# Kernel tuning notes

Hardware: AMD Instinct MI355X
Metric: run time of the kernel (lower is better)

## Reference

```python
import jax, jax.numpy as jnp
import numpy as np

PRE_NMS_LIMIT = 6000
PROPOSAL_COUNT = 1000
NMS_THRESHOLD = 0.7
BBOX_STD = jnp.array([0.1, 0.1, 0.2, 0.2], dtype=jnp.float32)
NEG = -1e9  # suppressed-score sentinel


def setup_inputs() -> dict:
    key = jax.random.key(0)
    k1, k2, k3, k4 = jax.random.split(key, 4)
    B, N = 8, 262144
    rpn_probs = jax.random.uniform(k1, (B, N, 2), dtype=jnp.float32)
    rpn_bbox = jax.random.normal(k2, (B, N, 4), dtype=jnp.float32) * 0.1
    # anchors as valid (y1, x1, y2, x2) boxes in normalized coords
    cyx = jax.random.uniform(k3, (B, N, 2), dtype=jnp.float32)
    hw = jax.random.uniform(k4, (B, N, 2), dtype=jnp.float32, minval=0.02, maxval=0.3)
    anchors = jnp.concatenate([cyx - 0.5 * hw, cyx + 0.5 * hw], axis=-1)
    return {"rpn_probs": rpn_probs, "rpn_bbox": rpn_bbox, "anchors": anchors}


def _apply_deltas(a, d):
    # a, d: [K, 4]; a = (y1, x1, y2, x2); d = (dy, dx, log dh, log dw)
    h = a[:, 2] - a[:, 0]
    w = a[:, 3] - a[:, 1]
    cy = a[:, 0] + 0.5 * h + d[:, 0] * h
    cx = a[:, 1] + 0.5 * w + d[:, 1] * w
    h = h * jnp.exp(d[:, 2])
    w = w * jnp.exp(d[:, 3])
    return jnp.stack([cy - 0.5 * h, cx - 0.5 * w, cy + 0.5 * h, cx + 0.5 * w], axis=-1)


def _iou_one_vs_all(box, boxes):
    # box [4], boxes [K, 4]
    y1 = jnp.maximum(box[0], boxes[:, 0])
    x1 = jnp.maximum(box[1], boxes[:, 1])
    y2 = jnp.minimum(box[2], boxes[:, 2])
    x2 = jnp.minimum(box[3], boxes[:, 3])
    inter = jnp.maximum(y2 - y1, 0.0) * jnp.maximum(x2 - x1, 0.0)
    area_b = (box[2] - box[0]) * (box[3] - box[1])
    areas = (boxes[:, 2] - boxes[:, 0]) * (boxes[:, 3] - boxes[:, 1])
    return inter / (area_b + areas - inter + 1e-10)


def _nms(boxes, scores):
    # greedy NMS: boxes [K, 4], scores [K] -> padded [P, 4], [P]
    K = scores.shape[0]
    idx = jnp.arange(K)

    def step(scores_m, _):
        i = jnp.argmax(scores_m)
        s = scores_m[i]
        valid = s > 0.5 * NEG
        box = boxes[i]
        iou = _iou_one_vs_all(box, boxes)
        scores_m = jnp.where((iou > NMS_THRESHOLD) | (idx == i), NEG, scores_m)
        return scores_m, (jnp.where(valid, box, 0.0), jnp.where(valid, s, 0.0))

    _, (props, pscores) = jax.lax.scan(step, scores, None, length=PROPOSAL_COUNT)
    return props, pscores


def reference(rpn_probs, rpn_bbox, anchors):
    scores = rpn_probs[:, :, 1]                      # [B, N] fg prob
    deltas = rpn_bbox * BBOX_STD                      # [B, N, 4]
    k = min(PRE_NMS_LIMIT, anchors.shape[1])
    top_scores, ix = jax.lax.top_k(scores, k)         # [B, K]
    gather = jax.vmap(lambda x, i: x[i])
    d = gather(deltas, ix)                            # [B, K, 4]
    a = gather(anchors, ix)                           # [B, K, 4]
    boxes = jax.vmap(_apply_deltas)(a, d)             # [B, K, 4]
    boxes = jnp.clip(boxes, 0.0, 1.0)                 # clip to window [0,0,1,1]
    proposals, pscores = jax.vmap(_nms)(boxes, top_scores)
    return proposals, pscores
```

## Files before the change

kernel.cpp:

```cpp
#include <hip/hip_runtime.h>
#include <stdint.h>

#define BB 8
#define NN 262144
#define KSEL 6000
#define KPAD2 6144
#define NW2 24
#define PROP 1000
#define NMS_THR 0.7f
#define CAND_CAP 8192
#define BPB 64
#define STAGE_CAP 768
#define MAT_U64_PB 282624ull
#define DIAG_U64_PB 24576ull

__device__ __forceinline__ unsigned long long shfl_xor_u64(unsigned long long v, int m) {
    unsigned lo = (unsigned)v, hi = (unsigned)(v >> 32);
    lo = __shfl_xor(lo, m);
    hi = __shfl_xor(hi, m);
    return ((unsigned long long)hi << 32) | lo;
}
__device__ __forceinline__ uint64_t rdfl64(uint64_t v) {
    uint32_t lo = __builtin_amdgcn_readfirstlane((uint32_t)v);
    uint32_t hi = __builtin_amdgcn_readfirstlane((uint32_t)(v >> 32));
    return ((uint64_t)hi << 32) | lo;
}
__device__ __forceinline__ uint64_t rdlane64(uint64_t v, uint32_t l) {
    uint32_t lo = __builtin_amdgcn_readlane((uint32_t)v, l);
    uint32_t hi = __builtin_amdgcn_readlane((uint32_t)(v >> 32), l);
    return ((uint64_t)hi << 32) | lo;
}

__device__ __forceinline__ uint32_t sup_bit(const float4 bi, float ai, const float4 bj, float aj) {
    float y1 = fmaxf(bi.x, bj.x), x1 = fmaxf(bi.y, bj.y);
    float y2 = fminf(bi.z, bj.z), x2 = fminf(bi.w, bj.w);
    float inter = __fmul_rn(fmaxf(__fsub_rn(y2, y1), 0.f), fmaxf(__fsub_rn(x2, x1), 0.f));
    float den = __fadd_rn(__fsub_rn(__fadd_rn(ai, aj), inter), 1e-10f);
    const double MSUP = 23488103.0 / 33554432.0;
    return (double)inter >= MSUP * (double)den;
}

__device__ __forceinline__ uint32_t score_bin(float sc) {
    uint32_t u = (uint32_t)(sc * 16777216.0f);
    u = u > 16777215u ? 16777215u : u;
    return u >> 16;
}

__global__ void k_zero(uint32_t* __restrict__ ghist, uint32_t* __restrict__ cnt,
                       uint32_t* __restrict__ ncount, uint32_t* __restrict__ ndone) {
    int b = blockIdx.x, t = threadIdx.x;
    ghist[(b << 8) + t] = 0u;
    if (t == 0) { cnt[b] = 0u; ncount[b] = 0u; ndone[b] = 0u; }
}

__global__ void k_hist(const float4* __restrict__ probs, uint32_t* __restrict__ ghist) {
    __shared__ uint32_t lh[256];
    int blk = blockIdx.x;
    int b = blk >> 6;
    int t = threadIdx.x;
    lh[t] = 0u;
    __syncthreads();
    size_t fbase = ((size_t)b * (NN / 2)) + (size_t)(blk & 63) * 2048;
#pragma unroll
    for (int k = 0; k < 8; ++k) {
        float4 v = probs[fbase + k * 256 + t];
        atomicAdd(&lh[score_bin(v.y)], 1u);
        atomicAdd(&lh[score_bin(v.w)], 1u);
    }
    __syncthreads();
    uint32_t c = lh[t];
    if (c) atomicAdd(&ghist[(b << 8) + t], c);
}

__global__ void k_compact(const float4* __restrict__ probs, const uint32_t* __restrict__ ghist,
                          uint32_t* __restrict__ cnt, uint64_t* __restrict__ cand) {
    __shared__ uint64_t stage[STAGE_CAP];
    __shared__ uint32_t lh[256];
    __shared__ uint32_t s_bst, lcnt, lbase;
    int blk = blockIdx.x;
    int b = blk >> 6;
    int t = threadIdx.x;
    lh[t] = ghist[(b << 8) + t];
    if (t == 0) lcnt = 0u;
    __syncthreads();
    if (t == 0) {
        uint32_t cum = 0; uint32_t bst = 0;
        for (int c = 255; c >= 0; --c) {
            cum += lh[c];
            if (cum >= (uint32_t)KSEL) { bst = (uint32_t)c; break; }
        }
        s_bst = bst;
    }
    __syncthreads();
    uint32_t bst = s_bst;
    int ibase = (blk & 63) * 4096;
    size_t fbase = ((size_t)b * (NN / 2)) + (size_t)(blk & 63) * 2048;
#pragma unroll
    for (int k = 0; k < 8; ++k) {
        float4 v = probs[fbase + k * 256 + t];
        int i0 = ibase + (k * 256 + t) * 2;
#pragma unroll
        for (int e = 0; e < 2; ++e) {
            float sc = e ? v.w : v.y;
            if (score_bin(sc) >= bst) {
                uint32_t p = atomicAdd(&lcnt, 1u);
                if (p < STAGE_CAP) {
                    uint32_t bits = __float_as_uint(sc);
                    stage[p] = ((uint64_t)bits << 32) | (uint32_t)(~(uint32_t)(i0 + e));
                }
            }
        }
    }
    __syncthreads();
    if (t == 0) {
        uint32_t m = lcnt > STAGE_CAP ? STAGE_CAP : lcnt;
        lbase = atomicAdd(&cnt[b], m);
        lcnt = m;
    }
    __syncthreads();
    uint32_t m = lcnt, base = lbase;
    for (uint32_t s = t; s < m; s += 256) {
        uint32_t pos = base + s;
        if (pos < CAND_CAP) cand[((uint64_t)b << 13) + pos] = stage[s];
    }
}

__launch_bounds__(512)
__global__ void k_sort1(const uint32_t* __restrict__ cnt, uint64_t* __restrict__ cand) {
    __shared__ uint64_t key[1024];
    int b = blockIdx.y, ch = blockIdx.x, t = threadIdx.x;
    uint32_t M = cnt[b]; if (M > CAND_CAP) M = CAND_CAP;
    uint64_t* cb = cand + ((uint64_t)b << 13);
    int base = ch << 10;
    for (int i = t; i < 1024; i += 512) key[i] = ((uint32_t)(base + i) < M) ? cb[base + i] : 0ull;
    __syncthreads();
    for (int kk = 2; kk <= 1024; kk <<= 1) {
        for (int j = kk >> 1; j > 0; j >>= 1) {
            for (int e = t; e < 1024; e += 512) {
                int ixj = e ^ j;
                if (ixj > e) {
                    uint64_t a = key[e], c = key[ixj];
                    bool ddd = ((e & kk) == 0);
                    if ((a < c) == ddd) { key[e] = c; key[ixj] = a; }
                }
            }
            __syncthreads();
        }
    }
    for (int i = t; i < 1024; i += 512) cb[base + i] = key[i];
}

__launch_bounds__(256)
__global__ void k_merge(int R, const uint64_t* __restrict__ src, uint64_t* __restrict__ dst) {
    int b = blockIdx.y;
    int k = (blockIdx.x << 8) + threadIdx.x;
    const uint64_t* base = src + ((uint64_t)b << 13);
    int run = k / (2 * R);
    int ko = k - run * (2 * R);
    const uint64_t* A = base + (size_t)run * 2 * R;
    const uint64_t* B = A + R;
    int lo = ko - R; if (lo < 0) lo = 0;
    int hi = ko < R ? ko : R;
    while (lo < hi) {
        int m = (lo + hi) >> 1;
        int t = ko - m - 1;
        uint64_t bv = (t < 0) ? ~0ull : (t >= R ? 0ull : B[t]);
        if (A[m] > bv) lo = m + 1; else hi = m;
    }
    int i = lo, j = ko - lo;
    uint64_t av = (i >= R) ? 0ull : A[i];
    uint64_t bv = (j >= R) ? 0ull : B[j];
    dst[((uint64_t)b << 13) + k] = (av > bv) ? av : bv;
}

__launch_bounds__(256)
__global__ void k_merge_decode(const uint64_t* __restrict__ src,
                               const float4* __restrict__ rpn_bbox, const float4* __restrict__ anchors,
                               float4* __restrict__ boxes, float* __restrict__ scoresS,
                               float* __restrict__ areas) {
    const int R = 4096;
    int b = blockIdx.y;
    int k = (blockIdx.x << 8) + threadIdx.x;
    if (k >= KPAD2) return;
    const uint64_t* A = src + ((uint64_t)b << 13);
    const uint64_t* B = A + R;
    int lo = k - R; if (lo < 0) lo = 0;
    int hi = k < R ? k : R;
    while (lo < hi) {
        int m = (lo + hi) >> 1;
        int t = k - m - 1;
        uint64_t bv = (t < 0) ? ~0ull : (t >= R ? 0ull : B[t]);
        if (A[m] > bv) lo = m + 1; else hi = m;
    }
    int i = lo, j = k - lo;
    uint64_t av = (i >= R) ? 0ull : A[i];
    uint64_t bv = (j >= R) ? 0ull : B[j];
    uint64_t k64 = (av > bv) ? av : bv;

    float4 bx = make_float4(0.f, 0.f, 0.f, 0.f);
    float sc = 0.f, ar = 0.f;
    if (k < KSEL) {
        uint32_t idx = ~(uint32_t)(k64 & 0xFFFFFFFFull);
        sc = __uint_as_float((uint32_t)(k64 >> 32));
        size_t off = ((size_t)b << 18) + idx;
        float4 a = anchors[off];
        float4 d4 = rpn_bbox[off];
        float d0 = __fmul_rn(d4.x, 0.1f), d1 = __fmul_rn(d4.y, 0.1f);
        float d2 = __fmul_rn(d4.z, 0.2f), d3 = __fmul_rn(d4.w, 0.2f);
        float h = __fsub_rn(a.z, a.x), w = __fsub_rn(a.w, a.y);
        float cy = __fadd_rn(__fadd_rn(a.x, __fmul_rn(0.5f, h)), __fmul_rn(d0, h));
        float cx = __fadd_rn(__fadd_rn(a.y, __fmul_rn(0.5f, w)), __fmul_rn(d1, w));
        float h2 = __fmul_rn(h, expf(d2));
        float w2 = __fmul_rn(w, expf(d3));
        float y1 = __fsub_rn(cy, __fmul_rn(0.5f, h2));
        float x1 = __fsub_rn(cx, __fmul_rn(0.5f, w2));
        float y2 = __fadd_rn(cy, __fmul_rn(0.5f, h2));
        float x2 = __fadd_rn(cx, __fmul_rn(0.5f, w2));
        y1 = fminf(fmaxf(y1, 0.f), 1.f); x1 = fminf(fmaxf(x1, 0.f), 1.f);
        y2 = fminf(fmaxf(y2, 0.f), 1.f); x2 = fminf(fmaxf(x2, 0.f), 1.f);
        bx = make_float4(y1, x1, y2, x2);
        ar = __fmul_rn(__fsub_rn(y2, y1), __fsub_rn(x2, x1));
    }
    boxes[b * KPAD2 + k] = bx;
    scoresS[b * KPAD2 + k] = sc;
    areas[b * KPAD2 + k] = ar;
}

__launch_bounds__(256)
__global__ void k_matc(int w0, const float4* __restrict__ boxes, const float* __restrict__ areas,
                       uint64_t* __restrict__ mat, uint64_t* __restrict__ diag,
                       const uint32_t* __restrict__ done) {
    int b = blockIdx.y;
    if (done[b]) return;
    int q2 = blockIdx.x;
    int half = q2 & 1;
    int q = q2 >> 1, W = w0;
    while (q >= W + 1) { q -= W + 1; ++W; }
    int sub = q;
    int t = threadIdx.x;
    __shared__ float4 sb[128];
    __shared__ float sa[128];
    size_t bb = (size_t)b * KPAD2;
    int j0 = (W << 8) + (half << 7);
    if (t < 128) { sb[t] = boxes[bb + j0 + t]; sa[t] = areas[bb + j0 + t]; }
    __syncthreads();
    int i = (sub << 8) + t;
    float4 bi = boxes[bb + i];
    float ai = areas[bb + i];
    uint32_t a0 = 0, a1 = 0, a2 = 0, a3 = 0;
#pragma unroll 4
    for (int jj = 0; jj < 32; ++jj) {
        a0 |= sup_bit(bi, ai, sb[jj], sa[jj]) << jj;
        a1 |= sup_bit(bi, ai, sb[32 + jj], sa[32 + jj]) << jj;
        a2 |= sup_bit(bi, ai, sb[64 + jj], sa[64 + jj]) << jj;
        a3 |= sup_bit(bi, ai, sb[96 + jj], sa[96 + jj]) << jj;
    }
    uint64_t* row;
    if (sub == W) {
        row = diag + (uint64_t)b * DIAG_U64_PB + (uint64_t)(j0 & ~127) * 0
              + (uint64_t)((W << 8) + t) * 4;
    } else {
        row = mat + (uint64_t)b * MAT_U64_PB + 512ull * W * (W - 1) + (uint64_t)i * 4;
    }
    ulonglong2 v;
    v.x = (uint64_t)a0 | ((uint64_t)a1 << 32);
    v.y = (uint64_t)a2 | ((uint64_t)a3 << 32);
    *(ulonglong2*)(row + (half << 1)) = v;
}

__launch_bounds__(256)
__global__ void k_nms_chunk(int w0, int w1, int final_chunk,
                            const float4* __restrict__ boxes, const float* __restrict__ scoresS,
                            const uint64_t* __restrict__ diag, const uint64_t* __restrict__ mat,
                            uint32_t* __restrict__ gsel, uint32_t* __restrict__ ncount,
                            uint32_t* __restrict__ done, float* __restrict__ out) {
    __shared__ uint32_t sel[PROP];
    __shared__ uint64_t diagrow[256][4];
    __shared__ uint32_t suppw[8];
    __shared__ uint32_t s_count;

    int b = blockIdx.x;
    if (done[b]) return;
    int tid = threadIdx.x;
    int wid = tid >> 6, lane = tid & 63;
    size_t bb = (size_t)b * KPAD2;
    const uint64_t* mb = mat + (uint64_t)b * MAT_U64_PB;
    const uint64_t* dgb = diag + (uint64_t)b * DIAG_U64_PB;
    uint32_t* gs = gsel + b * 1024;

    int count = (int)ncount[b];
    for (int r = tid; r < count; r += 256) sel[r] = gs[r];
    __syncthreads();

    for (int W = w0; W < w1; ++W) {
        {
            const ulonglong2* src = (const ulonglong2*)(dgb + (uint64_t)(W << 8) * 4);
            ulonglong2* dst = (ulonglong2*)&diagrow[0][0];
            dst[tid * 2] = src[tid * 2];
            dst[tid * 2 + 1] = src[tid * 2 + 1];
        }
        if (tid < 8) suppw[tid] = 0u;
        __syncthreads();
        uint64_t acc0 = 0, acc1 = 0, acc2 = 0, acc3 = 0;
        {
            const uint64_t* col = mb + 512ull * W * (W - 1);
            uint32_t c = (uint32_t)count;
            uint32_t i0 = tid, i1 = tid + 256, i2 = tid + 512, i3 = tid + 768;
            if (i0 < c) { const ulonglong2* r = (const ulonglong2*)(col + 4u * sel[i0]);
                          ulonglong2 x = r[0], y = r[1];
                          acc0 |= x.x; acc1 |= x.y; acc2 |= y.x; acc3 |= y.y; }
            if (i1 < c) { const ulonglong2* r = (const ulonglong2*)(col + 4u * sel[i1]);
                          ulonglong2 x = r[0], y = r[1];
                          acc0 |= x.x; acc1 |= x.y; acc2 |= y.x; acc3 |= y.y; }
            if (i2 < c) { const ulonglong2* r = (const ulonglong2*)(col + 4u * sel[i2]);
                          ulonglong2 x = r[0], y = r[1];
                          acc0 |= x.x; acc1 |= x.y; acc2 |= y.x; acc3 |= y.y; }
            if (i3 < c) { const ulonglong2* r = (const ulonglong2*)(col + 4u * sel[i3]);
                          ulonglong2 x = r[0], y = r[1];
                          acc0 |= x.x; acc1 |= x.y; acc2 |= y.x; acc3 |= y.y; }
        }
#pragma unroll
        for (int off = 32; off; off >>= 1) {
            acc0 |= shfl_xor_u64(acc0, off);
            acc1 |= shfl_xor_u64(acc1, off);
            acc2 |= shfl_xor_u64(acc2, off);
            acc3 |= shfl_xor_u64(acc3, off);
        }
        if (lane == 0) {
            if (acc0) { atomicOr(&suppw[0], (uint32_t)acc0); atomicOr(&suppw[1], (uint32_t)(acc0 >> 32)); }
            if (acc1) { atomicOr(&suppw[2], (uint32_t)acc1); atomicOr(&suppw[3], (uint32_t)(acc1 >> 32)); }
            if (acc2) { atomicOr(&suppw[4], (uint32_t)acc2); atomicOr(&suppw[5], (uint32_t)(acc2 >> 32)); }
            if (acc3) { atomicOr(&suppw[6], (uint32_t)acc3); atomicOr(&suppw[7], (uint32_t)(acc3 >> 32)); }
        }
        __syncthreads();
        int count_old = count;
        if (wid == 0) {
            uint64_t a0 = ~(((uint64_t)suppw[1] << 32) | suppw[0]);
            uint64_t a1 = ~(((uint64_t)suppw[3] << 32) | suppw[2]);
            uint64_t a2 = ~(((uint64_t)suppw[5] << 32) | suppw[4]);
            uint64_t a3 = ~(((uint64_t)suppw[7] << 32) | suppw[6]);
            if (W == NW2 - 1) { a1 &= (1ull << 48) - 1; a2 = 0; a3 = 0; }
            uint64_t pk0 = 0, pk1 = 0, pk2 = 0, pk3 = 0;
            uint64_t hi_mask = (lane == 63) ? 0ull : (~0ull << (lane + 1));

#define SUBP(S, AS, PK)                                                       \
            if (AS && count < PROP) {                                         \
                uint64_t own = diagrow[(S << 6) + lane][S];                   \
                while (AS && count < PROP) {                                  \
                    uint32_t alive_l = (uint32_t)((AS >> lane) & 1ull);       \
                    uint64_t inter = own & AS & hi_mask;                      \
                    unsigned long long conf = __ballot(alive_l && (inter != 0ull)); \
                    uint64_t run, rowc = 0ull;                                \
                    if (conf == 0ull) { run = AS; }                           \
                    else {                                                    \
                        uint32_t c = (uint32_t)__builtin_ctzll(conf);         \
                        uint64_t lo = ((1ull << c) << 1) - 1ull;              \
                        run = AS & lo;                                        \
                        rowc = rdlane64(own, c);                              \
                    }                                                         \
                    int pr = (int)__popcll(run);                              \
                    if (count + pr > PROP) {                                  \
                        int need = PROP - count;                              \
                        while (need-- > 0) {                                  \
                            uint32_t bp = (uint32_t)__builtin_ctzll(run);     \
                            PK |= 1ull << bp;                                 \
                            run &= run - 1ull;                                \
                        }                                                     \
                        count = PROP; AS = 0ull;                              \
                    } else {                                                  \
                        PK |= run; count += pr;                               \
                        AS &= ~run; AS &= ~rowc;                              \
                    }                                                         \
                }                                                             \
            }
            SUBP(0, a0, pk0)
            if (pk0 && count < PROP) {
                uint32_t pl = (uint32_t)((pk0 >> lane) & 1ull);
                uint64_t x1 = pl ? diagrow[lane][1] : 0ull;
                uint64_t x2 = pl ? diagrow[lane][2] : 0ull;
                uint64_t x3 = pl ? diagrow[lane][3] : 0ull;
#pragma unroll
                for (int off = 32; off; off >>= 1) {
                    x1 |= shfl_xor_u64(x1, off);
                    x2 |= shfl_xor_u64(x2, off);
                    x3 |= shfl_xor_u64(x3, off);
                }
                a1 &= ~rdfl64(x1); a2 &= ~rdfl64(x2); a3 &= ~rdfl64(x3);
            }
            SUBP(1, a1, pk1)
            if (pk1 && count < PROP) {
                uint32_t pl = (uint32_t)((pk1 >> lane) & 1ull);
                uint64_t x2 = pl ? diagrow[64 + lane][2] : 0ull;
                uint64_t x3 = pl ? diagrow[64 + lane][3] : 0ull;
#pragma unroll
                for (int off = 32; off; off >>= 1) {
                    x2 |= shfl_xor_u64(x2, off);
                    x3 |= shfl_xor_u64(x3, off);
                }
                a2 &= ~rdfl64(x2); a3 &= ~rdfl64(x3);
            }
            SUBP(2, a2, pk2)
            if (pk2 && count < PROP) {
                uint32_t pl = (uint32_t)((pk2 >> lane) & 1ull);
                uint64_t x3 = pl ? diagrow[128 + lane][3] : 0ull;
#pragma unroll
                for (int off = 32; off; off >>= 1) x3 |= shfl_xor_u64(x3, off);
                a3 &= ~rdfl64(x3);
            }
            SUBP(3, a3, pk3)
#undef SUBP
            uint32_t nb = (uint32_t)count_old;
#define APPEND(S, PK) {                                                       \
            if (PK) {                                                         \
                uint32_t my = (uint32_t)((PK >> lane) & 1ull);                \
                uint32_t rank = (uint32_t)__popcll(PK & ((1ull << lane) - 1ull));\
                if (my) {                                                     \
                    uint32_t v = (uint32_t)((W << 8) + (S << 6) + lane);      \
                    sel[nb + rank] = v;                                       \
                    gs[nb + rank] = v;                                        \
                }                                                             \
                nb += (uint32_t)__popcll(PK);                                 \
            } }
            APPEND(0, pk0)
            APPEND(1, pk1)
            APPEND(2, pk2)
            APPEND(3, pk3)
#undef APPEND
            if (lane == 0) s_count = (uint32_t)count;
        }
        __syncthreads();
        count = (int)s_count;
        if (count >= PROP) break;
    }

    if (count >= PROP || final_chunk) {
        if (tid == 0) { done[b] = 1u; ncount[b] = (uint32_t)count; }
        float* prop = out + b * (PROP * 4);
        float* psc = out + BB * PROP * 4 + b * PROP;
        for (int r = tid; r < PROP; r += 256) {
            if (r < count) {
                uint32_t j = sel[r];
                float4 bx = boxes[bb + j];
                *(float4*)(prop + r * 4) = bx;
                psc[r] = scoresS[bb + j];
            } else {
                *(float4*)(prop + r * 4) = make_float4(0.f, 0.f, 0.f, 0.f);
                psc[r] = 0.f;
            }
        }
    } else {
        if (tid == 0) ncount[b] = (uint32_t)count;
    }
}

extern "C" void kernel_launch(void* const* d_in, const int* in_sizes, int n_in,
                              void* d_out, int out_size, void* d_ws, size_t ws_size,
                              hipStream_t stream) {
    const float4* probs = (const float4*)d_in[0];
    const float4* rpn_bbox = (const float4*)d_in[1];
    const float4* anchors = (const float4*)d_in[2];
    float* out = (float*)d_out;

    uint8_t* p = (uint8_t*)d_ws;
    size_t off = 0;
    auto alloc = [&](size_t bytes) -> void* {
        void* q = p + off;
        off += (bytes + 255) & ~(size_t)255;
        return q;
    };
    uint32_t* ghist = (uint32_t*)alloc((size_t)BB * 256 * 4);
    uint32_t* cnt = (uint32_t*)alloc(BB * 4);
    uint32_t* ncount = (uint32_t*)alloc(BB * 4);
    uint32_t* ndone = (uint32_t*)alloc(BB * 4);
    uint64_t* cand = (uint64_t*)alloc((size_t)BB * CAND_CAP * 8);
    uint64_t* cand2 = (uint64_t*)alloc((size_t)BB * CAND_CAP * 8);
    float4* boxes = (float4*)alloc((size_t)BB * KPAD2 * 16);
    float* scoresS = (float*)alloc((size_t)BB * KPAD2 * 4);
    float* areas = (float*)alloc((size_t)BB * KPAD2 * 4);
    uint32_t* gsel = (uint32_t*)alloc((size_t)BB * 1024 * 4);
    uint64_t* diag = (uint64_t*)alloc((size_t)BB * DIAG_U64_PB * 8);
    uint64_t* mat = (uint64_t*)alloc((size_t)BB * MAT_U64_PB * 8);

    if (off > ws_size) {
        hipMemsetAsync(d_out, 0, (size_t)out_size * 4, stream);
        return;
    }

    k_zero<<<BB, 256, 0, stream>>>(ghist, cnt, ncount, ndone);

    k_hist<<<BB * BPB, 256, 0, stream>>>(probs, ghist);
    k_compact<<<BB * BPB, 256, 0, stream>>>(probs, ghist, cnt, cand);
    dim3 gs1(8, BB);
    k_sort1<<<gs1, 512, 0, stream>>>(cnt, cand);
    dim3 gmg(32, BB);
    k_merge<<<gmg, 256, 0, stream>>>(1024, cand, cand2);
    k_merge<<<gmg, 256, 0, stream>>>(2048, cand2, cand);
    dim3 gmd(24, BB);
    k_merge_decode<<<gmd, 256, 0, stream>>>(cand, rpn_bbox, anchors, boxes, scoresS, areas);

    const int cb[3] = {0, 6, 24};
    for (int c = 0; c < 2; ++c) {
        int w0 = cb[c], w1 = cb[c + 1];
        int nblk = 0;
        for (int W = w0; W < w1; ++W) nblk += W + 1;
        dim3 gm(nblk * 2, BB);
        k_matc<<<gm, 256, 0, stream>>>(w0, boxes, areas, mat, diag, ndone);
        k_nms_chunk<<<BB, 256, 0, stream>>>(w0, w1, (w1 == NW2) ? 1 : 0,
                                            boxes, scoresS, diag, mat,
                                            gsel, ncount, ndone, out);
    }
}
```

Baseline: 101.6 us.

## Remove zero kernel via per-block histograms and fuse two merge passes

```diff
diff --git a/kernel.cpp b/kernel.cpp
--- a/kernel.cpp
+++ b/kernel.cpp
@@ -46,19 +46,15 @@
     return u >> 16;
 }
 
-__global__ void k_zero(uint32_t* __restrict__ ghist, uint32_t* __restrict__ cnt,
-                       uint32_t* __restrict__ ncount, uint32_t* __restrict__ ndone) {
-    int b = blockIdx.x, t = threadIdx.x;
-    ghist[(b << 8) + t] = 0u;
-    if (t == 0) { cnt[b] = 0u; ncount[b] = 0u; ndone[b] = 0u; }
-}
-
-__global__ void k_hist(const float4* __restrict__ probs, uint32_t* __restrict__ ghist) {
+__global__ void k_hist(const float4* __restrict__ probs, uint32_t* __restrict__ bhist,
+                       uint32_t* __restrict__ cnt, uint32_t* __restrict__ ncount,
+                       uint32_t* __restrict__ ndone) {
     __shared__ uint32_t lh[256];
     int blk = blockIdx.x;
     int b = blk >> 6;
     int t = threadIdx.x;
     lh[t] = 0u;
+    if (blk == 0 && t < BB) { cnt[t] = 0u; ncount[t] = 0u; ndone[t] = 0u; }
     __syncthreads();
     size_t fbase = ((size_t)b * (NN / 2)) + (size_t)(blk & 63) * 2048;
 #pragma unroll
@@ -68,11 +64,10 @@
         atomicAdd(&lh[score_bin(v.w)], 1u);
     }
     __syncthreads();
-    uint32_t c = lh[t];
-    if (c) atomicAdd(&ghist[(b << 8) + t], c);
-}
-
-__global__ void k_compact(const float4* __restrict__ probs, const uint32_t* __restrict__ ghist,
+    bhist[((size_t)b << 14) + ((size_t)(blk & 63) << 8) + t] = lh[t];
+}
+
+__global__ void k_compact(const float4* __restrict__ probs, const uint32_t* __restrict__ bhist,
                           uint32_t* __restrict__ cnt, uint64_t* __restrict__ cand) {
     __shared__ uint64_t stage[STAGE_CAP];
     __shared__ uint32_t lh[256];
@@ -80,7 +75,13 @@
     int blk = blockIdx.x;
     int b = blk >> 6;
     int t = threadIdx.x;
-    lh[t] = ghist[(b << 8) + t];
+    {
+        const uint32_t* bh = bhist + ((size_t)b << 14);
+        uint32_t s = 0;
+#pragma unroll 8
+        for (int k = 0; k < 64; ++k) s += bh[(k << 8) + t];
+        lh[t] = s;
+    }
     if (t == 0) lcnt = 0u;
     __syncthreads();
     if (t == 0) {
@@ -150,27 +151,50 @@
     for (int i = t; i < 1024; i += 512) cb[base + i] = key[i];
 }
 
-__launch_bounds__(256)
-__global__ void k_merge(int R, const uint64_t* __restrict__ src, uint64_t* __restrict__ dst) {
-    int b = blockIdx.y;
-    int k = (blockIdx.x << 8) + threadIdx.x;
-    const uint64_t* base = src + ((uint64_t)b << 13);
-    int run = k / (2 * R);
-    int ko = k - run * (2 * R);
-    const uint64_t* A = base + (size_t)run * 2 * R;
-    const uint64_t* B = A + R;
-    int lo = ko - R; if (lo < 0) lo = 0;
-    int hi = ko < R ? ko : R;
-    while (lo < hi) {
-        int m = (lo + hi) >> 1;
-        int t = ko - m - 1;
-        uint64_t bv = (t < 0) ? ~0ull : (t >= R ? 0ull : B[t]);
-        if (A[m] > bv) lo = m + 1; else hi = m;
-    }
-    int i = lo, j = ko - lo;
-    uint64_t av = (i >= R) ? 0ull : A[i];
-    uint64_t bv = (j >= R) ? 0ull : B[j];
-    dst[((uint64_t)b << 13) + k] = (av > bv) ? av : bv;
+__launch_bounds__(512)
+__global__ void k_merge2(const uint64_t* __restrict__ src, uint64_t* __restrict__ dst) {
+    __shared__ uint64_t k1[4096];
+    __shared__ uint64_t k2[4096];
+    int b = blockIdx.y, seg = blockIdx.x, t = threadIdx.x;
+    const uint64_t* base = src + ((uint64_t)b << 13) + (size_t)seg * 4096;
+    for (int i = t; i < 4096; i += 512) k1[i] = base[i];
+    __syncthreads();
+    for (int o = t; o < 4096; o += 512) {
+        int pair = o >> 11;
+        int ko = o & 2047;
+        const uint64_t* A = k1 + (pair << 11);
+        const uint64_t* B = A + 1024;
+        int lo = ko - 1024; if (lo < 0) lo = 0;
+        int hi = ko < 1024 ? ko : 1024;
+        while (lo < hi) {
+            int m = (lo + hi) >> 1;
+            int tt = ko - m - 1;
+            uint64_t bv = (tt < 0) ? ~0ull : (tt >= 1024 ? 0ull : B[tt]);
+            if (A[m] > bv) lo = m + 1; else hi = m;
+        }
+        int i = lo, j = ko - lo;
+        uint64_t av = (i >= 1024) ? 0ull : A[i];
+        uint64_t bv = (j >= 1024) ? 0ull : B[j];
+        k2[o] = (av > bv) ? av : bv;
+    }
+    __syncthreads();
+    uint64_t* outp = dst + ((uint64_t)b << 13) + (size_t)seg * 4096;
+    for (int o = t; o < 4096; o += 512) {
+        const uint64_t* A = k2;
+        const uint64_t* B = k2 + 2048;
+        int lo = o - 2048; if (lo < 0) lo = 0;
+        int hi = o < 2048 ? o : 2048;
+        while (lo < hi) {
+            int m = (lo + hi) >> 1;
+            int tt = o - m - 1;
+            uint64_t bv = (tt < 0) ? ~0ull : (tt >= 2048 ? 0ull : B[tt]);
+            if (A[m] > bv) lo = m + 1; else hi = m;
+        }
+        int i = lo, j = o - lo;
+        uint64_t av = (i >= 2048) ? 0ull : A[i];
+        uint64_t bv = (j >= 2048) ? 0ull : B[j];
+        outp[o] = (av > bv) ? av : bv;
+    }
 }
 
 __launch_bounds__(256)
@@ -257,8 +281,7 @@
     }
     uint64_t* row;
     if (sub == W) {
-        row = diag + (uint64_t)b * DIAG_U64_PB + (uint64_t)(j0 & ~127) * 0
-              + (uint64_t)((W << 8) + t) * 4;
+        row = diag + (uint64_t)b * DIAG_U64_PB + (uint64_t)((W << 8) + t) * 4;
     } else {
         row = mat + (uint64_t)b * MAT_U64_PB + 512ull * W * (W - 1) + (uint64_t)i * 4;
     }
@@ -468,7 +491,7 @@
         off += (bytes + 255) & ~(size_t)255;
         return q;
     };
-    uint32_t* ghist = (uint32_t*)alloc((size_t)BB * 256 * 4);
+    uint32_t* bhist = (uint32_t*)alloc((size_t)BB * 64 * 256 * 4);
     uint32_t* cnt = (uint32_t*)alloc(BB * 4);
     uint32_t* ncount = (uint32_t*)alloc(BB * 4);
     uint32_t* ndone = (uint32_t*)alloc(BB * 4);
@@ -486,17 +509,14 @@
         return;
     }
 
-    k_zero<<<BB, 256, 0, stream>>>(ghist, cnt, ncount, ndone);
-
-    k_hist<<<BB * BPB, 256, 0, stream>>>(probs, ghist);
-    k_compact<<<BB * BPB, 256, 0, stream>>>(probs, ghist, cnt, cand);
+    k_hist<<<BB * BPB, 256, 0, stream>>>(probs, bhist, cnt, ncount, ndone);
+    k_compact<<<BB * BPB, 256, 0, stream>>>(probs, bhist, cnt, cand);
     dim3 gs1(8, BB);
     k_sort1<<<gs1, 512, 0, stream>>>(cnt, cand);
-    dim3 gmg(32, BB);
-    k_merge<<<gmg, 256, 0, stream>>>(1024, cand, cand2);
-    k_merge<<<gmg, 256, 0, stream>>>(2048, cand2, cand);
+    dim3 gm2(2, BB);
+    k_merge2<<<gm2, 512, 0, stream>>>(cand, cand2);
     dim3 gmd(24, BB);
-    k_merge_decode<<<gmd, 256, 0, stream>>>(cand, rpn_bbox, anchors, boxes, scoresS, areas);
+    k_merge_decode<<<gmd, 256, 0, stream>>>(cand2, rpn_bbox, anchors, boxes, scoresS, areas);
 
     const int cb[3] = {0, 6, 24};
     for (int c = 0; c < 2; ++c) {
```

Measured after the change: 111.2 us. 1.09x slower.
